# Kernel tuning notes

Hardware: AMD Instinct MI355X
Metric: run time of the kernel (lower is better)

Reference implementation:

```python
import jax, jax.numpy as jnp
import numpy as np

N, D, S, E, EL, ITERS = 250_000, 128, 6, 500_000, 50_000, 4


def setup_inputs() -> dict:
    key = jax.random.key(0)
    ks = jax.random.split(key, 16)
    s = 1.0 / np.sqrt(D)  # keep activations O(1)
    return {
        'feat':   jax.random.normal(ks[0], (N, D), jnp.float32),
        'pre_u':  jax.random.randint(ks[1], (S, E), 0, N, jnp.int32),
        'pre_v':  jax.random.randint(ks[2], (S, E), 0, N, jnp.int32),
        'suc_u':  jax.random.randint(ks[3], (S, E), 0, N, jnp.int32),
        'suc_v':  jax.random.randint(ks[4], (S, E), 0, N, jnp.int32),
        'left_u': jax.random.randint(ks[5], (EL,), 0, N, jnp.int32),
        'left_v': jax.random.randint(ks[6], (EL,), 0, N, jnp.int32),
        'right_u': jax.random.randint(ks[7], (EL,), 0, N, jnp.int32),
        'right_v': jax.random.randint(ks[8], (EL,), 0, N, jnp.int32),
        'W_ctr':   jax.random.normal(ks[9],  (ITERS, D, D), jnp.float32) * s,
        'W_pre':   jax.random.normal(ks[10], (ITERS, S, D, D), jnp.float32) * s,
        'W_suc':   jax.random.normal(ks[11], (ITERS, S, D, D), jnp.float32) * s,
        'W_left':  jax.random.normal(ks[12], (ITERS, D, D), jnp.float32) * s,
        'W_right': jax.random.normal(ks[13], (ITERS, D, D), jnp.float32) * s,
        'gn1_w': jnp.ones((ITERS, D), jnp.float32),
        'gn1_b': jnp.zeros((ITERS, D), jnp.float32),
        'W_ctr2':  jax.random.normal(ks[14], (ITERS, D, D), jnp.float32) * s,
        'gn2_w': jnp.ones((ITERS, D), jnp.float32),
        'gn2_b': jnp.zeros((ITERS, D), jnp.float32),
    }


def _gn(x, w, b, eps=1e-5):
    # torch GroupNorm(1, D) on a [N, D] input: per-row normalization over channels
    mu = jnp.mean(x, -1, keepdims=True)
    var = jnp.mean((x - mu) ** 2, -1, keepdims=True)
    return (x - mu) * jax.lax.rsqrt(var + eps) * w + b


def reference(feat, pre_u, pre_v, suc_u, suc_v, left_u, left_v, right_u, right_v,
              W_ctr, W_pre, W_suc, W_left, W_right, gn1_w, gn1_b,
              W_ctr2, gn2_w, gn2_b):
    res = feat
    for i in range(ITERS):  # 4 fusion iterations, structurally distinct weights
        temp = feat @ W_ctr[i].T  # nn.Linear(bias=False): x @ W.T
        for k in range(S):  # 6 dilation scales, pre and suc edges
            temp = temp.at[pre_u[k]].add(feat[pre_v[k]] @ W_pre[i, k].T)
            temp = temp.at[suc_u[k]].add(feat[suc_v[k]] @ W_suc[i, k].T)
        temp = temp.at[left_u].add(feat[left_v] @ W_left[i].T)
        temp = temp.at[right_u].add(feat[right_v] @ W_right[i].T)
        h = jax.nn.relu(_gn(temp, gn1_w[i], gn1_b[i]))           # fuse['norm'] + relu
        h = _gn(h @ W_ctr2[i].T, gn2_w[i], gn2_b[i])             # fuse['ctr2']: Linear+GN, no act
        feat = jax.nn.relu(h + res)                              # residual + relu
        res = feat
    return feat
```

## Files before the change

kernel.cpp:

```cpp
#include <hip/hip_runtime.h>


#define NN 250000
#define DD 128
#define EE 500000
#define ELE 50000
#define NITER 4
#define NL 14
#define M14 (NL*NN)
#define TOTE (12*EE + 2*ELE)
#define KBIG (15*DD)
#define BK 64
#define TILES_TOTAL ((NN + 127)/128)
#define NBKT TILES_TOTAL
#define BCAP 4096
#define LK (128*NL)
#define NBLK_BUCKET 256
#define EPB ((TOTE + NBLK_BUCKET - 1)/NBLK_BUCKET)

typedef unsigned short u16;
typedef __attribute__((ext_vector_type(4))) float f32x4;
typedef __attribute__((ext_vector_type(8))) __bf16 bf16x8;

static __device__ __forceinline__ unsigned f2bf(float f) {
  unsigned u = __float_as_uint(f);
  return (u + 0x7fffu + ((u >> 16) & 1u)) >> 16;
}
static __device__ __forceinline__ float bflo(unsigned w){ return __uint_as_float(w << 16); }
static __device__ __forceinline__ float bfhi(unsigned w){ return __uint_as_float(w & 0xffff0000u); }

static __device__ __forceinline__ void gload16(const u16* g, u16* l) {
  __builtin_amdgcn_global_load_lds(
      (const __attribute__((address_space(1))) void*)g,
      (__attribute__((address_space(3))) void*)l, 16, 0, 0);
}

static __device__ __forceinline__ int edge_u(int idx,
    const int* __restrict__ pu, const int* __restrict__ su,
    const int* __restrict__ lu, const int* __restrict__ ru) {
  if (idx < 12*EE) {
    int l = idx / EE; int e = idx - l*EE;
    return (l < 6) ? pu[l*EE + e] : su[(l-6)*EE + e];
  }
  int r = idx - 12*EE;
  return (r < ELE) ? lu[r] : ru[r - ELE];
}

static __device__ __forceinline__ void edge_luv(int idx,
    const int* __restrict__ pu, const int* __restrict__ pv,
    const int* __restrict__ su, const int* __restrict__ sv,
    const int* __restrict__ lu, const int* __restrict__ lv,
    const int* __restrict__ ru, const int* __restrict__ rv,
    int& l, int& u, int& v) {
  if (idx < 12*EE) {
    l = idx / EE; int e = idx - l*EE;
    if (l < 6) { u = pu[l*EE+e]; v = pv[l*EE+e]; }
    else       { u = su[(l-6)*EE+e]; v = sv[(l-6)*EE+e]; }
  } else {
    int r = idx - 12*EE;
    if (r < ELE) { l = 12; u = lu[r]; v = lv[r]; }
    else         { l = 13; u = ru[r-ELE]; v = rv[r-ELE]; }
  }
}

__global__ __launch_bounds__(1024) void k_bucket(
    const int* __restrict__ pu, const int* __restrict__ pv,
    const int* __restrict__ su, const int* __restrict__ sv,
    const int* __restrict__ lu, const int* __restrict__ lv,
    const int* __restrict__ ru, const int* __restrict__ rv,
    int* __restrict__ bcur, unsigned* __restrict__ bstage) {
  __shared__ int cnt[NBKT];
  __shared__ int cur[NBKT];
  int t = threadIdx.x;
  for (int i=t; i<NBKT; i+=1024) cnt[i] = 0;
  __syncthreads();
  int e0 = blockIdx.x * EPB;
  int e1 = e0 + EPB; if (e1 > TOTE) e1 = TOTE;
  for (int idx = e0 + t; idx < e1; idx += 1024) {
    int u = edge_u(idx, pu, su, lu, ru);
    atomicAdd(&cnt[u >> 7], 1);
  }
  __syncthreads();
  for (int i=t; i<NBKT; i+=1024) {
    int c = cnt[i];
    cur[i] = c ? atomicAdd(&bcur[i], c) : 0;
  }
  __syncthreads();
  for (int idx = e0 + t; idx < e1; idx += 1024) {
    int l, u, v;
    edge_luv(idx, pu, pv, su, sv, lu, lv, ru, rv, l, u, v);
    int b = u >> 7;
    unsigned rec = ((unsigned)((u & 127)*NL + l) << 18) | (unsigned)v;
    int pos = atomicAdd(&cur[b], 1);
    if (pos < BCAP) bstage[(size_t)b*BCAP + pos] = rec;
  }
}

__global__ void k_bscan(const int* __restrict__ bcur, int* __restrict__ bbase,
                        int* __restrict__ rowptr) {
  __shared__ int wsum[4];
  int t = threadIdx.x, lane = t & 63, w = t >> 6;
  int v[8]; int s = 0;
  #pragma unroll
  for (int j=0;j<8;j++){
    int idx = t*8 + j;
    int x = 0;
    if (idx < NBKT) { x = bcur[idx]; if (x > BCAP) x = BCAP; }
    v[j] = s; s += x;
  }
  int ps = s;
  for (int d=1; d<64; d<<=1) { int o = __shfl_up(ps, d); if (lane >= d) ps += o; }
  if (lane == 63) wsum[w] = ps;
  __syncthreads();
  int woff = 0;
  for (int j=0;j<w;j++) woff += wsum[j];
  int excl = woff + ps - s;
  #pragma unroll
  for (int j=0;j<8;j++){
    int idx = t*8 + j;
    if (idx < NBKT) bbase[idx] = excl + v[j];
  }
  if (t == 255) rowptr[M14] = excl + s;
}

__global__ __launch_bounds__(256) void k_place(const unsigned* __restrict__ bstage,
    const int* __restrict__ bcur, const int* __restrict__ bbase,
    int* __restrict__ rowptr, int* __restrict__ edge_v) {
  __shared__ int lh[LK];
  __shared__ int lex[LK];
  __shared__ int wsum[4];
  int b = blockIdx.x, t = threadIdx.x;
  int lane = t & 63, w = t >> 6;
  int cnt = bcur[b]; if (cnt > BCAP) cnt = BCAP;
  int base = bbase[b];
  const unsigned* rec = bstage + (size_t)b*BCAP;
  for (int i=t; i<LK; i+=256) lh[i] = 0;
  __syncthreads();
  for (int e=t; e<cnt; e+=256) atomicAdd(&lh[rec[e]>>18], 1);
  __syncthreads();
  int s = 0;
  int my[7];
  #pragma unroll
  for (int j=0;j<7;j++){ my[j] = s; s += lh[t*7+j]; }
  int ps = s;
  for (int d=1; d<64; d<<=1) { int o = __shfl_up(ps, d); if (lane >= d) ps += o; }
  if (lane == 63) wsum[w] = ps;
  __syncthreads();
  int woff = 0;
  for (int j=0;j<w;j++) woff += wsum[j];
  int excl = woff + ps - s;
  #pragma unroll
  for (int j=0;j<7;j++) lex[t*7+j] = excl + my[j];
  __syncthreads();
  for (int i=t; i<LK; i+=256) rowptr[(size_t)b*LK + i] = base + lex[i];
  for (int i=t; i<LK; i+=256) lh[i] = lex[i];
  __syncthreads();
  for (int e=t; e<cnt; e+=256) {
    unsigned r = rec[e];
    int pos = atomicAdd(&lh[r>>18], 1);
    edge_v[base + pos] = (int)(r & 0x3FFFFu);
  }
}

__global__ void k_f2bf(const float* __restrict__ in, unsigned* __restrict__ out) {
  int i = blockIdx.x*256 + threadIdx.x;
  float2 v = ((const float2*)in)[i];
  out[i] = f2bf(v.x) | (f2bf(v.y) << 16);
}

__global__ void k_bw(const float* __restrict__ Wc, const float* __restrict__ Wp,
                     const float* __restrict__ Ws, const float* __restrict__ Wl,
                     const float* __restrict__ Wr, const float* __restrict__ Wc2,
                     int it, u16* __restrict__ wcat, u16* __restrict__ wc2) {
  int i = blockIdx.x*256 + threadIdx.x;
  if (i < 128*KBIG) {
    int r = i / KBIG, K = i - r*KBIG;
    int s = K >> 7, c = K & 127;
    float val;
    if (s == 0)       val = Wc[(it*128 + r)*128 + c];
    else if (s <= 6)  val = Wp[((it*6 + (s-1))*128 + r)*128 + c];
    else if (s <= 12) val = Ws[((it*6 + (s-7))*128 + r)*128 + c];
    else if (s == 13) val = Wl[(it*128 + r)*128 + c];
    else              val = Wr[(it*128 + r)*128 + c];
    wcat[i] = (u16)f2bf(val);
  } else {
    int j = i - 128*KBIG;
    wc2[j] = (u16)f2bf(Wc2[it*16384 + j]);
  }
}

__global__ __launch_bounds__(256) void k_agg(const unsigned* __restrict__ featbf,
    const int* __restrict__ rowptr, const int* __restrict__ edge_v,
    unsigned* __restrict__ X, int chunk_base) {
  int wid = threadIdx.x >> 6, lane = threadIdx.x & 63;
  int nl = blockIdx.x*4 + wid;
  int node = chunk_base + nl;
  size_t xb = (size_t)nl * (14*64);
  if (node >= NN) {
    #pragma unroll
    for (int s=0;s<14;s++) X[xb + s*64 + lane] = 0;
    return;
  }
  int rp = 0;
  if (lane < 15) rp = rowptr[node*NL + lane];
  int st0 = __shfl(rp, 0);
  int cnt = __shfl(rp, 14) - st0;
  float ax = 0.f, ay = 0.f;
  int s = 0;
  int nextb = __shfl(rp, 1);
  int vv = 0;
  for (int base = 0; base < cnt; base += 16) {
    int off = base & 63;
    if (off == 0) vv = edge_v[st0 + base + lane];
    int m = cnt - base; if (m > 16) m = 16;
    unsigned wrow[16];
    #pragma unroll
    for (int q=0;q<16;q++) if (q < m) {
      int v = __shfl(vv, off + q);
      wrow[q] = featbf[(size_t)v*64 + lane];
    }
    #pragma unroll
    for (int q=0;q<16;q++) if (q < m) {
      int e = st0 + base + q;
      while (e == nextb && s < 14) {
        X[xb + s*64 + lane] = f2bf(ax) | (f2bf(ay) << 16);
        ax = 0.f; ay = 0.f; s++;
        int ni = s + 1; if (ni > 14) ni = 14;
        nextb = __shfl(rp, ni);
      }
      ax += bflo(wrow[q]); ay += bfhi(wrow[q]);
    }
  }
  while (s < 14) {
    X[xb + s*64 + lane] = f2bf(ax) | (f2bf(ay) << 16);
    ax = 0.f; ay = 0.f; s++;
  }
}

__global__ __launch_bounds__(256) void gemm_fused(
    const u16* __restrict__ Xc, const unsigned* __restrict__ fbf,
    const u16* __restrict__ Bw, const u16* __restrict__ wc2g,
    unsigned* __restrict__ fout, float* __restrict__ out32, int last,
    const float* __restrict__ g1w, const float* __restrict__ g1b,
    const float* __restrict__ g2w, const float* __restrict__ g2b,
    int row0_abs) {
  __shared__ u16 smem[2*128*BK];
  __shared__ float stats[2][128][2];
  u16* As = smem; u16* Bs = smem + 128*BK;
  int tid = threadIdx.x, wid = tid >> 6, lane = tid & 63;
  int wm = wid >> 1, wn = wid & 1;
  int g = lane >> 4, l15 = lane & 15, l7 = lane & 7;
  int tile_row = blockIdx.x * 128;
  f32x4 acc[4][4] = {};
  int srow8 = lane >> 3;
  int scol = ((lane & 7) ^ srow8) * 8;
  for (int k0 = 0; k0 < KBIG; k0 += BK) {
    __syncthreads();
    if (k0 < DD) {
      #pragma unroll
      for (int j=0;j<4;j++) {
        int seg = wid + j*4; int r = seg*8 + srow8;
        int arow = row0_abs + tile_row + r; if (arow > NN-1) arow = NN-1;
        gload16((const u16*)fbf + (size_t)arow*DD + (k0 + scol), &As[seg*512]);
        gload16(Bw + (size_t)r*KBIG + (k0 + scol), &Bs[seg*512]);
      }
    } else {
      #pragma unroll
      for (int j=0;j<4;j++) {
        int seg = wid + j*4; int r = seg*8 + srow8;
        gload16(Xc + (size_t)(tile_row + r)*(14*128) + (k0 - DD + scol), &As[seg*512]);
        gload16(Bw + (size_t)r*KBIG + (k0 + scol), &Bs[seg*512]);
      }
    }
    __syncthreads();
    #pragma unroll
    for (int kk=0; kk<2; kk++) {
      bf16x8 af[4], bfr[4];
      #pragma unroll
      for (int mt=0; mt<4; mt++)
        af[mt] = *(const bf16x8*)&As[((wm*64 + mt*16 + l15)*BK + kk*32 + g*8) ^ (l7<<3)];
      #pragma unroll
      for (int nt=0; nt<4; nt++)
        bfr[nt] = *(const bf16x8*)&Bs[((wn*64 + nt*16 + l15)*BK + kk*32 + g*8) ^ (l7<<3)];
      #pragma unroll
      for (int mt=0; mt<4; mt++)
        #pragma unroll
        for (int nt=0; nt<4; nt++)
          acc[mt][nt] = __builtin_amdgcn_mfma_f32_16x16x32_bf16(af[mt], bfr[nt], acc[mt][nt], 0, 0, 0);
    }
  }
  __syncthreads();

  #pragma unroll
  for (int mt=0; mt<4; mt++)
    #pragma unroll
    for (int r=0; r<4; r++) {
      float s = 0.f, q = 0.f;
      #pragma unroll
      for (int nt=0; nt<4; nt++) { float v = acc[mt][nt][r]; s += v; q += v*v; }
      #pragma unroll
      for (int d=1; d<16; d<<=1) { s += __shfl_xor(s, d); q += __shfl_xor(q, d); }
      if (l15 == 0) {
        int R = wm*64 + mt*16 + g*4 + r;
        stats[wn][R][0] = s; stats[wn][R][1] = q;
      }
    }
  __syncthreads();

  float w1[4], b1[4], w2[4], b2[4];
  #pragma unroll
  for (int nt=0; nt<4; nt++) {
    int C = wn*64 + nt*16 + l15;
    w1[nt] = g1w[C]; b1[nt] = g1b[C];
    w2[nt] = g2w[C]; b2[nt] = g2b[C];
  }
  #pragma unroll
  for (int mt=0; mt<4; mt++)
    #pragma unroll
    for (int r=0; r<4; r++) {
      int R = wm*64 + mt*16 + g*4 + r;
      float ts = stats[0][R][0] + stats[1][R][0];
      float tq = stats[0][R][1] + stats[1][R][1];
      float mu = ts*(1.f/DD), var = tq*(1.f/DD) - mu*mu;
      float rs = rsqrtf(var + 1e-5f);
      #pragma unroll
      for (int nt=0; nt<4; nt++) {
        int C = wn*64 + nt*16 + l15;
        float y = fmaxf(fmaf((acc[mt][nt][r]-mu)*rs, w1[nt], b1[nt]), 0.f);
        float p = __shfl_xor(y, 1);
        if (!(lane & 1)) {
          unsigned word = f2bf(y) | (f2bf(p) << 16);
          *(unsigned*)&smem[(R*128 + (C & ~1)) ^ ((R&7)<<3)] = word;
        }
      }
    }
  __syncthreads();

  f32x4 a2[4][4] = {};
  #pragma unroll
  for (int kk2=0; kk2<4; kk2++) {
    bf16x8 wf[4], hf[4];
    #pragma unroll
    for (int nt=0; nt<4; nt++)
      wf[nt] = *(const bf16x8*)&wc2g[(size_t)(wn*64 + nt*16 + l15)*DD + kk2*32 + g*8];
    #pragma unroll
    for (int mt=0; mt<4; mt++)
      hf[mt] = *(const bf16x8*)&smem[((wm*64 + mt*16 + l15)*128 + kk2*32 + g*8) ^ (l7<<3)];
    #pragma unroll
    for (int mt=0; mt<4; mt++)
      #pragma unroll
      for (int nt=0; nt<4; nt++)
        a2[mt][nt] = __builtin_amdgcn_mfma_f32_16x16x32_bf16(hf[mt], wf[nt], a2[mt][nt], 0, 0, 0);
  }
  __syncthreads();

  #pragma unroll
  for (int mt=0; mt<4; mt++)
    #pragma unroll
    for (int r=0; r<4; r++) {
      float s = 0.f, q = 0.f;
      #pragma unroll
      for (int nt=0; nt<4; nt++) { float v = a2[mt][nt][r]; s += v; q += v*v; }
      #pragma unroll
      for (int d=1; d<16; d<<=1) { s += __shfl_xor(s, d); q += __shfl_xor(q, d); }
      if (l15 == 0) {
        int R = wm*64 + mt*16 + g*4 + r;
        stats[wn][R][0] = s; stats[wn][R][1] = q;
      }
    }
  __syncthreads();

  #pragma unroll
  for (int mt=0; mt<4; mt++)
    #pragma unroll
    for (int r=0; r<4; r++) {
      int R = wm*64 + mt*16 + g*4 + r;
      int grow = row0_abs + tile_row + R;
      float ts = stats[0][R][0] + stats[1][R][0];
      float tq = stats[0][R][1] + stats[1][R][1];
      float mu = ts*(1.f/DD), var = tq*(1.f/DD) - mu*mu;
      float rs = rsqrtf(var + 1e-5f);
      bool ok = grow < NN;
      #pragma unroll
      for (int nt=0; nt<4; nt++) {
        int C = wn*64 + nt*16 + l15;
        float yv = fmaf((a2[mt][nt][r]-mu)*rs, w2[nt], b2[nt]);
        unsigned rw = ok ? fbf[(size_t)grow*64 + (C>>1)] : 0u;
        float resv = (lane & 1) ? bfhi(rw) : bflo(rw);
        float o = fmaxf(yv + resv, 0.f);
        if (last && ok) out32[(size_t)grow*DD + C] = o;
        float p = __shfl_xor(o, 1);
        if (!(lane & 1) && ok)
          fout[(size_t)grow*64 + (C>>1)] = f2bf(o) | (f2bf(p) << 16);
      }
    }
}

extern "C" void kernel_launch(void* const* d_in, const int* in_sizes, int n_in,
                              void* d_out, int out_size, void* d_ws, size_t ws_size,
                              hipStream_t stream) {
  const float* feat_in = (const float*)d_in[0];
  const int* pre_u  = (const int*)d_in[1];
  const int* pre_v  = (const int*)d_in[2];
  const int* suc_u  = (const int*)d_in[3];
  const int* suc_v  = (const int*)d_in[4];
  const int* left_u = (const int*)d_in[5];
  const int* left_v = (const int*)d_in[6];
  const int* right_u= (const int*)d_in[7];
  const int* right_v= (const int*)d_in[8];
  const float* W_ctr  = (const float*)d_in[9];
  const float* W_pre  = (const float*)d_in[10];
  const float* W_suc  = (const float*)d_in[11];
  const float* W_left = (const float*)d_in[12];
  const float* W_right= (const float*)d_in[13];
  const float* gn1w   = (const float*)d_in[14];
  const float* gn1b   = (const float*)d_in[15];
  const float* W_ctr2 = (const float*)d_in[16];
  const float* gn2w   = (const float*)d_in[17];
  const float* gn2b   = (const float*)d_in[18];

  char* ws = (char*)d_ws;
  size_t off = 0;
  auto alloc = [&](size_t bytes) -> char* {
    char* p = ws + off; off += (bytes + 255) & ~(size_t)255; return p;
  };
  unsigned* featA  = (unsigned*)alloc((size_t)NN*64*4);
  unsigned* featB  = (unsigned*)alloc((size_t)NN*64*4);
  u16*      wcat   = (u16*)     alloc((size_t)128*KBIG*2);
  u16*      wc2    = (u16*)     alloc((size_t)128*128*2);
  int*      rowptr = (int*)     alloc(((size_t)NBKT*LK + 1)*4);
  int*      edge_v = (int*)     alloc((size_t)(TOTE + 64)*4);
  unsigned* bstage = (unsigned*)alloc((size_t)NBKT*BCAP*4);
  int*      bcur   = (int*)     alloc((size_t)NBKT*4);
  int*      bbase  = (int*)     alloc((size_t)NBKT*4);

  size_t tile_bytes = (size_t)128*(14*128)*2;
  size_t avail = (ws_size > off + 65536) ? (ws_size - off - 65536) : 0;
  int chunk_tiles = (int)(avail / tile_bytes);
  if (chunk_tiles > 256) chunk_tiles = 256;
  if (chunk_tiles < 8) chunk_tiles = 8;
  u16* Xc = (u16*)alloc((size_t)chunk_tiles * tile_bytes);
  int nchunk = (TILES_TOTAL + chunk_tiles - 1) / chunk_tiles;
  (void)in_sizes; (void)n_in; (void)out_size;

  (void)hipMemsetAsync(bcur, 0, (size_t)NBKT*4, stream);
  k_bucket<<<NBLK_BUCKET, 1024, 0, stream>>>(pre_u, pre_v, suc_u, suc_v,
                                             left_u, left_v, right_u, right_v,
                                             bcur, bstage);
  k_bscan<<<1, 256, 0, stream>>>(bcur, bbase, rowptr);
  k_place<<<NBKT, 256, 0, stream>>>(bstage, bcur, bbase, rowptr, edge_v);

  k_f2bf<<<NN*64/256, 256, 0, stream>>>(feat_in, featA);

  for (int it = 0; it < NITER; it++) {
    unsigned* fin = (it & 1) ? featB : featA;
    unsigned* fo  = (it & 1) ? featA : featB;
    int last = (it == NITER-1) ? 1 : 0;
    k_bw<<<1024, 256, 0, stream>>>(W_ctr, W_pre, W_suc, W_left, W_right, W_ctr2, it, wcat, wc2);
    for (int c = 0; c < nchunk; c++) {
      int tile0 = c*chunk_tiles;
      int tiles = (TILES_TOTAL - tile0 < chunk_tiles) ? (TILES_TOTAL - tile0) : chunk_tiles;
      int base  = tile0*128;
      k_agg<<<tiles*32, 256, 0, stream>>>(fin, rowptr, edge_v, (unsigned*)Xc, base);
      gemm_fused<<<tiles, 256, 0, stream>>>((const u16*)Xc, fin, wcat, wc2,
                                            fo, (float*)d_out, last,
                                            gn1w + it*DD, gn1b + it*DD,
                                            gn2w + it*DD, gn2b + it*DD, base);
    }
  }
}
```

Measured before the change: 4.721 ms.

## Software-pipeline aggregation and GEMM chunks in a single mixed kernel

Merges the gather-aggregation kernel and the fused GEMM into one launch. Each launch aggregates chunk d into one of two ping-pong buffers while GEMM blocks, interleaved at a fixed stride, consume chunk d-1 from the other buffer. The aim is to overlap the memory-bound gather with the MFMA-bound GEMM and to cut the number of kernel launches. In exchange, each buffer gets half the workspace, which may mean more chunks, and aggregation and GEMM blocks with very different resource needs now share one kernel.

```diff
diff --git a/kernel.cpp b/kernel.cpp
--- a/kernel.cpp
+++ b/kernel.cpp
@@ -189,68 +189,74 @@
   }
 }
 
-__global__ __launch_bounds__(256) void k_agg(const unsigned* __restrict__ featbf,
+__global__ __launch_bounds__(256) void k_mix(
+    const u16* __restrict__ Xr, unsigned* __restrict__ Xw,
+    const unsigned* __restrict__ fbf,
+    const u16* __restrict__ Bw, const u16* __restrict__ wc2g,
     const int* __restrict__ rowptr, const int* __restrict__ edge_v,
-    unsigned* __restrict__ X, int chunk_base) {
-  int wid = threadIdx.x >> 6, lane = threadIdx.x & 63;
-  int nl = blockIdx.x*4 + wid;
-  int node = chunk_base + nl;
-  size_t xb = (size_t)nl * (14*64);
-  if (node >= NN) {
-    #pragma unroll
-    for (int s=0;s<14;s++) X[xb + s*64 + lane] = 0;
-    return;
-  }
-  int rp = 0;
-  if (lane < 15) rp = rowptr[node*NL + lane];
-  int st0 = __shfl(rp, 0);
-  int cnt = __shfl(rp, 14) - st0;
-  float ax = 0.f, ay = 0.f;
-  int s = 0;
-  int nextb = __shfl(rp, 1);
-  int vv = 0;
-  for (int base = 0; base < cnt; base += 16) {
-    int off = base & 63;
-    if (off == 0) vv = edge_v[st0 + base + lane];
-    int m = cnt - base; if (m > 16) m = 16;
-    unsigned wrow[16];
-    #pragma unroll
-    for (int q=0;q<16;q++) if (q < m) {
-      int v = __shfl(vv, off + q);
-      wrow[q] = featbf[(size_t)v*64 + lane];
-    }
-    #pragma unroll
-    for (int q=0;q<16;q++) if (q < m) {
-      int e = st0 + base + q;
-      while (e == nextb && s < 14) {
-        X[xb + s*64 + lane] = f2bf(ax) | (f2bf(ay) << 16);
-        ax = 0.f; ay = 0.f; s++;
-        int ni = s + 1; if (ni > 14) ni = 14;
-        nextb = __shfl(rp, ni);
-      }
-      ax += bflo(wrow[q]); ay += bfhi(wrow[q]);
-    }
-  }
-  while (s < 14) {
-    X[xb + s*64 + lane] = f2bf(ax) | (f2bf(ay) << 16);
-    ax = 0.f; ay = 0.f; s++;
-  }
-}
-
-__global__ __launch_bounds__(256) void gemm_fused(
-    const u16* __restrict__ Xc, const unsigned* __restrict__ fbf,
-    const u16* __restrict__ Bw, const u16* __restrict__ wc2g,
     unsigned* __restrict__ fout, float* __restrict__ out32, int last,
     const float* __restrict__ g1w, const float* __restrict__ g1b,
     const float* __restrict__ g2w, const float* __restrict__ g2b,
-    int row0_abs) {
+    int base_g, int base_a, int nG, int stride) {
   __shared__ u16 smem[2*128*BK];
   __shared__ float stats[2][128][2];
+  int b = blockIdx.x;
+  int tid = threadIdx.x, wid = tid >> 6, lane = tid & 63;
+  bool is_g = (nG > 0) && (b % stride == 0) && (b / stride < nG);
+
+  if (!is_g) {
+    int g_before = (nG > 0) ? ((b + stride - 1) / stride) : 0;
+    if (g_before > nG) g_before = nG;
+    int aid = b - g_before;
+    int nl = aid*4 + wid;
+    int node = base_a + nl;
+    size_t xb = (size_t)nl * (14*64);
+    if (node >= NN) {
+      #pragma unroll
+      for (int s=0;s<14;s++) Xw[xb + s*64 + lane] = 0;
+      return;
+    }
+    int rp = 0;
+    if (lane < 15) rp = rowptr[node*NL + lane];
+    int st0 = __shfl(rp, 0);
+    int cnt = __shfl(rp, 14) - st0;
+    float ax = 0.f, ay = 0.f;
+    int s = 0;
+    int nextb = __shfl(rp, 1);
+    int vv = 0;
+    for (int base = 0; base < cnt; base += 16) {
+      int off = base & 63;
+      if (off == 0) vv = edge_v[st0 + base + lane];
+      int m = cnt - base; if (m > 16) m = 16;
+      unsigned wrow[16];
+      #pragma unroll
+      for (int q=0;q<16;q++) if (q < m) {
+        int v = __shfl(vv, off + q);
+        wrow[q] = fbf[(size_t)v*64 + lane];
+      }
+      #pragma unroll
+      for (int q=0;q<16;q++) if (q < m) {
+        int e = st0 + base + q;
+        while (e == nextb && s < 14) {
+          Xw[xb + s*64 + lane] = f2bf(ax) | (f2bf(ay) << 16);
+          ax = 0.f; ay = 0.f; s++;
+          int ni = s + 1; if (ni > 14) ni = 14;
+          nextb = __shfl(rp, ni);
+        }
+        ax += bflo(wrow[q]); ay += bfhi(wrow[q]);
+      }
+    }
+    while (s < 14) {
+      Xw[xb + s*64 + lane] = f2bf(ax) | (f2bf(ay) << 16);
+      ax = 0.f; ay = 0.f; s++;
+    }
+    return;
+  }
+
   u16* As = smem; u16* Bs = smem + 128*BK;
-  int tid = threadIdx.x, wid = tid >> 6, lane = tid & 63;
   int wm = wid >> 1, wn = wid & 1;
   int g = lane >> 4, l15 = lane & 15, l7 = lane & 7;
-  int tile_row = blockIdx.x * 128;
+  int tile_row = (b / stride) * 128;
   f32x4 acc[4][4] = {};
   int srow8 = lane >> 3;
   int scol = ((lane & 7) ^ srow8) * 8;
@@ -260,7 +266,7 @@
       #pragma unroll
       for (int j=0;j<4;j++) {
         int seg = wid + j*4; int r = seg*8 + srow8;
-        int arow = row0_abs + tile_row + r; if (arow > NN-1) arow = NN-1;
+        int arow = base_g + tile_row + r; if (arow > NN-1) arow = NN-1;
         gload16((const u16*)fbf + (size_t)arow*DD + (k0 + scol), &As[seg*512]);
         gload16(Bw + (size_t)r*KBIG + (k0 + scol), &Bs[seg*512]);
       }
@@ -268,7 +274,7 @@
       #pragma unroll
       for (int j=0;j<4;j++) {
         int seg = wid + j*4; int r = seg*8 + srow8;
-        gload16(Xc + (size_t)(tile_row + r)*(14*128) + (k0 - DD + scol), &As[seg*512]);
+        gload16(Xr + (size_t)(tile_row + r)*(14*128) + (k0 - DD + scol), &As[seg*512]);
         gload16(Bw + (size_t)r*KBIG + (k0 + scol), &Bs[seg*512]);
       }
     }
@@ -375,7 +381,7 @@
     #pragma unroll
     for (int r=0; r<4; r++) {
       int R = wm*64 + mt*16 + g*4 + r;
-      int grow = row0_abs + tile_row + R;
+      int grow = base_g + tile_row + R;
       float ts = stats[0][R][0] + stats[1][R][0];
       float tq = stats[0][R][1] + stats[1][R][1];
       float mu = ts*(1.f/DD), var = tq*(1.f/DD) - mu*mu;
@@ -436,10 +442,11 @@
 
   size_t tile_bytes = (size_t)128*(14*128)*2;
   size_t avail = (ws_size > off + 65536) ? (ws_size - off - 65536) : 0;
-  int chunk_tiles = (int)(avail / tile_bytes);
+  int chunk_tiles = (int)(avail / (2*tile_bytes));
   if (chunk_tiles > 256) chunk_tiles = 256;
   if (chunk_tiles < 8) chunk_tiles = 8;
-  u16* Xc = (u16*)alloc((size_t)chunk_tiles * tile_bytes);
+  unsigned* XcA = (unsigned*)alloc((size_t)chunk_tiles * tile_bytes);
+  unsigned* XcB = (unsigned*)alloc((size_t)chunk_tiles * tile_bytes);
   int nchunk = (TILES_TOTAL + chunk_tiles - 1) / chunk_tiles;
   (void)in_sizes; (void)n_in; (void)out_size;
 
@@ -457,15 +464,31 @@
     unsigned* fo  = (it & 1) ? featA : featB;
     int last = (it == NITER-1) ? 1 : 0;
     k_bw<<<1024, 256, 0, stream>>>(W_ctr, W_pre, W_suc, W_left, W_right, W_ctr2, it, wcat, wc2);
-    for (int c = 0; c < nchunk; c++) {
-      int tile0 = c*chunk_tiles;
-      int tiles = (TILES_TOTAL - tile0 < chunk_tiles) ? (TILES_TOTAL - tile0) : chunk_tiles;
-      int base  = tile0*128;
-      k_agg<<<tiles*32, 256, 0, stream>>>(fin, rowptr, edge_v, (unsigned*)Xc, base);
-      gemm_fused<<<tiles, 256, 0, stream>>>((const u16*)Xc, fin, wcat, wc2,
-                                            fo, (float*)d_out, last,
-                                            gn1w + it*DD, gn1b + it*DD,
-                                            gn2w + it*DD, gn2b + it*DD, base);
-    }
-  }
-}
+    for (int d = 0; d <= nchunk; d++) {
+      int cg = d - 1;
+      int ca = d;
+      int nG = 0, nA_tiles = 0;
+      if (cg >= 0) {
+        int t0 = cg*chunk_tiles;
+        nG = (TILES_TOTAL - t0 < chunk_tiles) ? (TILES_TOTAL - t0) : chunk_tiles;
+      }
+      if (ca < nchunk) {
+        int t0 = ca*chunk_tiles;
+        nA_tiles = (TILES_TOTAL - t0 < chunk_tiles) ? (TILES_TOTAL - t0) : chunk_tiles;
+      }
+      int nA = nA_tiles * 32;
+      int total = nG + nA;
+      if (total == 0) continue;
+      int stride = nG ? (total / nG) : 1;
+      if (stride < 1) stride = 1;
+      unsigned* Xw = (d & 1) ? XcB : XcA;
+      const u16* Xr = (const u16*)((d & 1) ? XcA : XcB);
+      k_mix<<<total, 256, 0, stream>>>(Xr, Xw, fin, wcat, wc2, rowptr, edge_v,
+                                       fo, (float*)d_out, last,
+                                       gn1w + it*DD, gn1b + it*DD,
+                                       gn2w + it*DD, gn2b + it*DD,
+                                       cg*chunk_tiles*128, ca*chunk_tiles*128,
+                                       nG, stride);
+    }
+  }
+}
```

Result: slower. 10.39 ms (+120.1%).

## Load GEMM operands directly from global into registers instead of staging through LDS

Applied to the files above, without the earlier changes.

The main fused GEMM no longer stages A and B tiles in LDS with global_load_lds and barriers. Each wave now reads its MFMA fragments straight from global memory using precomputed row pointers, with a separate loop for the feature part and for the 14-level aggregate part. This removes the per-K-step syncthreads and LDS traffic. In exchange, operands shared across waves are fetched redundantly from global or L2, and the 16-byte row-strided reads coalesce less well.

```diff
diff --git a/kernel.cpp b/kernel.cpp
--- a/kernel.cpp
+++ b/kernel.cpp
@@ -10,7 +10,6 @@
 #define M14 (NL*NN)
 #define TOTE (12*EE + 2*ELE)
 #define KBIG (15*DD)
-#define BK 64
 #define TILES_TOTAL ((NN + 127)/128)
 #define NBKT TILES_TOTAL
 #define BCAP 4096
@@ -28,12 +27,6 @@
 }
 static __device__ __forceinline__ float bflo(unsigned w){ return __uint_as_float(w << 16); }
 static __device__ __forceinline__ float bfhi(unsigned w){ return __uint_as_float(w & 0xffff0000u); }
-
-static __device__ __forceinline__ void gload16(const u16* g, u16* l) {
-  __builtin_amdgcn_global_load_lds(
-      (const __attribute__((address_space(1))) void*)g,
-      (__attribute__((address_space(3))) void*)l, 16, 0, 0);
-}
 
 static __device__ __forceinline__ int edge_u(int idx,
     const int* __restrict__ pu, const int* __restrict__ su,
@@ -244,52 +237,52 @@
     const float* __restrict__ g1w, const float* __restrict__ g1b,
     const float* __restrict__ g2w, const float* __restrict__ g2b,
     int row0_abs) {
-  __shared__ u16 smem[2*128*BK];
+  __shared__ u16 hbuf[128*128];
   __shared__ float stats[2][128][2];
-  u16* As = smem; u16* Bs = smem + 128*BK;
   int tid = threadIdx.x, wid = tid >> 6, lane = tid & 63;
   int wm = wid >> 1, wn = wid & 1;
   int g = lane >> 4, l15 = lane & 15, l7 = lane & 7;
   int tile_row = blockIdx.x * 128;
+
+  const u16* arF[4]; const u16* arX[4]; const u16* br[4];
+  #pragma unroll
+  for (int mt=0; mt<4; mt++) {
+    int lr = tile_row + wm*64 + mt*16 + l15;
+    int gr = row0_abs + lr; if (gr > NN-1) gr = NN-1;
+    arF[mt] = (const u16*)fbf + (size_t)gr*DD + g*8;
+    arX[mt] = Xc + (size_t)lr*(14*128) + g*8;
+  }
+  #pragma unroll
+  for (int nt=0; nt<4; nt++)
+    br[nt] = Bw + (size_t)(wn*64 + nt*16 + l15)*KBIG + g*8;
+
   f32x4 acc[4][4] = {};
-  int srow8 = lane >> 3;
-  int scol = ((lane & 7) ^ srow8) * 8;
-  for (int k0 = 0; k0 < KBIG; k0 += BK) {
-    __syncthreads();
-    if (k0 < DD) {
-      #pragma unroll
-      for (int j=0;j<4;j++) {
-        int seg = wid + j*4; int r = seg*8 + srow8;
-        int arow = row0_abs + tile_row + r; if (arow > NN-1) arow = NN-1;
-        gload16((const u16*)fbf + (size_t)arow*DD + (k0 + scol), &As[seg*512]);
-        gload16(Bw + (size_t)r*KBIG + (k0 + scol), &Bs[seg*512]);
-      }
-    } else {
-      #pragma unroll
-      for (int j=0;j<4;j++) {
-        int seg = wid + j*4; int r = seg*8 + srow8;
-        gload16(Xc + (size_t)(tile_row + r)*(14*128) + (k0 - DD + scol), &As[seg*512]);
-        gload16(Bw + (size_t)r*KBIG + (k0 + scol), &Bs[seg*512]);
-      }
-    }
-    __syncthreads();
-    #pragma unroll
-    for (int kk=0; kk<2; kk++) {
-      bf16x8 af[4], bfr[4];
-      #pragma unroll
-      for (int mt=0; mt<4; mt++)
-        af[mt] = *(const bf16x8*)&As[((wm*64 + mt*16 + l15)*BK + kk*32 + g*8) ^ (l7<<3)];
+  #pragma unroll
+  for (int ks=0; ks<4; ks++) {
+    bf16x8 af[4], bf[4];
+    #pragma unroll
+    for (int mt=0; mt<4; mt++) af[mt] = *(const bf16x8*)(arF[mt] + ks*32);
+    #pragma unroll
+    for (int nt=0; nt<4; nt++) bf[nt] = *(const bf16x8*)(br[nt] + ks*32);
+    #pragma unroll
+    for (int mt=0; mt<4; mt++)
       #pragma unroll
       for (int nt=0; nt<4; nt++)
-        bfr[nt] = *(const bf16x8*)&Bs[((wn*64 + nt*16 + l15)*BK + kk*32 + g*8) ^ (l7<<3)];
-      #pragma unroll
-      for (int mt=0; mt<4; mt++)
-        #pragma unroll
-        for (int nt=0; nt<4; nt++)
-          acc[mt][nt] = __builtin_amdgcn_mfma_f32_16x16x32_bf16(af[mt], bfr[nt], acc[mt][nt], 0, 0, 0);
-    }
-  }
-  __syncthreads();
+        acc[mt][nt] = __builtin_amdgcn_mfma_f32_16x16x32_bf16(af[mt], bf[nt], acc[mt][nt], 0, 0, 0);
+  }
+  #pragma unroll 2
+  for (int ks=0; ks<56; ks++) {
+    bf16x8 af[4], bf[4];
+    #pragma unroll
+    for (int mt=0; mt<4; mt++) af[mt] = *(const bf16x8*)(arX[mt] + ks*32);
+    #pragma unroll
+    for (int nt=0; nt<4; nt++) bf[nt] = *(const bf16x8*)(br[nt] + 128 + ks*32);
+    #pragma unroll
+    for (int mt=0; mt<4; mt++)
+      #pragma unroll
+      for (int nt=0; nt<4; nt++)
+        acc[mt][nt] = __builtin_amdgcn_mfma_f32_16x16x32_bf16(af[mt], bf[nt], acc[mt][nt], 0, 0, 0);
+  }
 
   #pragma unroll
   for (int mt=0; mt<4; mt++)
@@ -330,7 +323,7 @@
         float p = __shfl_xor(y, 1);
         if (!(lane & 1)) {
           unsigned word = f2bf(y) | (f2bf(p) << 16);
-          *(unsigned*)&smem[(R*128 + (C & ~1)) ^ ((R&7)<<3)] = word;
+          *(unsigned*)&hbuf[(R*128 + (C & ~1)) ^ ((R&7)<<3)] = word;
         }
       }
     }
@@ -345,7 +338,7 @@
       wf[nt] = *(const bf16x8*)&wc2g[(size_t)(wn*64 + nt*16 + l15)*DD + kk2*32 + g*8];
     #pragma unroll
     for (int mt=0; mt<4; mt++)
-      hf[mt] = *(const bf16x8*)&smem[((wm*64 + mt*16 + l15)*128 + kk2*32 + g*8) ^ (l7<<3)];
+      hf[mt] = *(const bf16x8*)&hbuf[((wm*64 + mt*16 + l15)*128 + kk2*32 + g*8) ^ (l7<<3)];
     #pragma unroll
     for (int mt=0; mt<4; mt++)
       #pragma unroll
```

New measurement: 5.722 ms. 21.2% more time.
